# Kernel tuning notes

Hardware: AMD Instinct MI355X
Metric: run time of the kernel (lower is better)

The kernel has to match this reference:

```python
import jax, jax.numpy as jnp
import numpy as np

N, E = 20000, 320000          # nodes, edges
R, B = 9, 9                   # num_relations, num_bases
IN, HID, OUT = 128, 256, 64   # feature dims
EPS = 1e-5                    # LayerNorm eps


def layer_norm(h, gamma, beta):
    mu = jnp.mean(h, axis=-1, keepdims=True)
    var = jnp.var(h, axis=-1, keepdims=True)
    return (h - mu) * jax.lax.rsqrt(var + EPS) * gamma + beta


def rgcn_conv(x, src, dst, etype, bases, comp, root, bias, aggr):
    # basis decomposition: W_r = sum_b comp[r,b] * bases[b]
    W = jnp.einsum('rb,bio->rio', comp, bases)          # [R, in, out]
    xW = jnp.einsum('ni,rio->rno', x, W)                # [R, N, out]
    msg = xW[etype, src]                                # [E, out] gather per edge
    if aggr == 'max':
        agg = jax.ops.segment_max(msg, dst, num_segments=N)
        agg = jnp.where(jnp.isfinite(agg), agg, 0.0)    # empty segments -> 0
    else:
        agg = jax.ops.segment_sum(msg, dst, num_segments=N)
    return agg + x @ root + bias


def setup_inputs() -> dict:
    key = jax.random.key(0)
    ks = jax.random.split(key, 12)
    rn = lambda k, s, sc=0.05: jax.random.normal(k, s, jnp.float32) * sc
    return {
        'x': jax.random.normal(ks[0], (N, IN), jnp.float32),
        'edge_index': jax.random.randint(ks[1], (2, E), 0, N),
        'edge_type': jax.random.randint(ks[2], (E,), 0, R),
        # conv1 params
        'bases1': rn(ks[3], (B, IN, HID)),
        'comp1': rn(ks[4], (R, B), 0.3),
        'root1': rn(ks[5], (IN, HID)),
        'bias1': jnp.zeros((HID,), jnp.float32),
        'g1': jnp.ones((HID,), jnp.float32),
        'b1': jnp.zeros((HID,), jnp.float32),
        # conv2 params
        'bases2': rn(ks[6], (B, HID, OUT)),
        'comp2': rn(ks[7], (R, B), 0.3),
        'root2': rn(ks[8], (HID, OUT)),
        'bias2': jnp.zeros((OUT,), jnp.float32),
        'g2': jnp.ones((OUT,), jnp.float32),
        'b2': jnp.zeros((OUT,), jnp.float32),
    }


def reference(x, edge_index, edge_type, bases1, comp1, root1, bias1, g1, b1,
              bases2, comp2, root2, bias2, g2, b2):
    src, dst = edge_index[0], edge_index[1]
    h = rgcn_conv(x, src, dst, edge_type, bases1, comp1, root1, bias1, 'max')
    h = jax.nn.relu(layer_norm(h, g1, b1))
    # eval mode: edge dropout and feature dropout are identity
    h = rgcn_conv(h, src, dst, edge_type, bases2, comp2, root2, bias2, 'add')
    h = layer_norm(h, g2, b2)
    return jax.nn.log_softmax(h, axis=1)
```

## Files before the change

### kernel.cpp

```cpp
#include <hip/hip_runtime.h>
#include <math.h>

#define NN 20000
#define NE 320000
#define NREL 9
#define NBASES 9
#define D_IN 128
#define D_HID 256
#define D_OUT 64
#define LN_EPS 1e-5f

#define N1 (NREL * D_HID + D_HID)
#define N2 (NREL * D_OUT + D_OUT)
#define NBLK ((NN + 255) / 256)

typedef __attribute__((ext_vector_type(8))) short bf16x8;
typedef __attribute__((ext_vector_type(4))) float f32x4;
typedef __attribute__((ext_vector_type(4))) unsigned int u32x4;

__device__ inline ushort f2b(float f) {
    unsigned u = __float_as_uint(f);
    return (ushort)((u + 0x7FFFu + ((u >> 16) & 1u)) >> 16);
}
__device__ inline float b2f(ushort h) { return __uint_as_float(((unsigned)h) << 16); }
__device__ inline float b2f_lo(unsigned u) { return __uint_as_float(u << 16); }
__device__ inline float b2f_hi(unsigned u) { return __uint_as_float(u & 0xffff0000u); }
__device__ inline unsigned pack2bf(float f0, float f1) {
    return (unsigned)f2b(f0) | ((unsigned)f2b(f1) << 16);
}

__global__ __launch_bounds__(256) void prep_all(
    const float* __restrict__ bases1, const float* __restrict__ comp1, const float* __restrict__ root1,
    const float* __restrict__ bases2, const float* __restrict__ comp2, const float* __restrict__ root2,
    const float* __restrict__ x, const int* __restrict__ dst,
    ushort* __restrict__ w1t, ushort* __restrict__ w2t, ushort* __restrict__ xbf,
    int* __restrict__ deg)
{
    const int SZW1 = D_IN * D_HID;
    const int SZW2 = D_HID * D_OUT;
    const int SZX4 = NN * D_IN / 4;
    int tid = blockIdx.x * 256 + threadIdx.x;
    if (tid < SZW1) {
        int o = tid & (D_HID - 1), k = tid >> 8;
        float acc[NREL];
        #pragma unroll
        for (int r = 0; r < NREL; r++) acc[r] = 0.f;
        #pragma unroll
        for (int b = 0; b < NBASES; b++) {
            float bs = bases1[(b * D_IN + k) * D_HID + o];
            #pragma unroll
            for (int r = 0; r < NREL; r++) acc[r] += comp1[r * NBASES + b] * bs;
        }
        #pragma unroll
        for (int r = 0; r < NREL; r++)
            w1t[(r * D_HID + o) * D_IN + k] = f2b(acc[r]);
        w1t[(NREL * D_HID + o) * D_IN + k] = f2b(root1[k * D_HID + o]);
    } else if (tid < SZW1 + SZW2) {
        int j = tid - SZW1;
        int o = j & (D_OUT - 1), k = j >> 6;
        float acc[NREL];
        #pragma unroll
        for (int r = 0; r < NREL; r++) acc[r] = 0.f;
        #pragma unroll
        for (int b = 0; b < NBASES; b++) {
            float bs = bases2[(b * D_HID + k) * D_OUT + o];
            #pragma unroll
            for (int r = 0; r < NREL; r++) acc[r] += comp2[r * NBASES + b] * bs;
        }
        #pragma unroll
        for (int r = 0; r < NREL; r++)
            w2t[(r * D_OUT + o) * D_HID + k] = f2b(acc[r]);
        w2t[(NREL * D_OUT + o) * D_HID + k] = f2b(root2[k * D_OUT + o]);
    } else if (tid < SZW1 + SZW2 + SZX4) {
        int j = tid - SZW1 - SZW2;
        float4 v = *(const float4*)&x[(size_t)j * 4];
        ushort4 o;
        o.x = f2b(v.x); o.y = f2b(v.y); o.z = f2b(v.z); o.w = f2b(v.w);
        *(ushort4*)&xbf[(size_t)j * 4] = o;
    } else if (tid < SZW1 + SZW2 + SZX4 + NE) {
        int e = tid - SZW1 - SZW2 - SZX4;
        atomicAdd(&deg[dst[e]], 1);
    }
}

__global__ __launch_bounds__(256) void scan_blk(
    const int* __restrict__ deg, int* __restrict__ local, int* __restrict__ bsum)
{
    __shared__ int wsum[4];
    int tid = threadIdx.x, lane = tid & 63, w = tid >> 6;
    int i = blockIdx.x * 256 + tid;
    int v = (i < NN) ? deg[i] : 0;
    int x = v;
    #pragma unroll
    for (int d = 1; d < 64; d <<= 1) {
        int y = __shfl_up(x, d, 64);
        if (lane >= d) x += y;
    }
    if (lane == 63) wsum[w] = x;
    __syncthreads();
    int woff = 0;
    for (int j = 0; j < w; j++) woff += wsum[j];
    if (i < NN) local[i] = woff + x - v;
    if (tid == 255) bsum[blockIdx.x] = woff + x;
}

__global__ __launch_bounds__(256) void scan_fin(
    const int* __restrict__ local, const int* __restrict__ bsum,
    int* __restrict__ offs, int* __restrict__ cursor)
{
    __shared__ int boff_s[NBLK];
    int tid = threadIdx.x;
    if (tid < 64) {
        int carry = 0;
        for (int base = 0; base < NBLK; base += 64) {
            int i = base + tid;
            int v = (i < NBLK) ? bsum[i] : 0;
            int x = v;
            #pragma unroll
            for (int d = 1; d < 64; d <<= 1) {
                int y = __shfl_up(x, d, 64);
                if (tid >= d) x += y;
            }
            if (i < NBLK) boff_s[i] = carry + x - v;
            carry += __shfl(x, 63, 64);
        }
    }
    __syncthreads();
    int i = blockIdx.x * 256 + tid;
    if (i < NN) {
        int o = local[i] + boff_s[i >> 8];
        offs[i] = o;
        cursor[i] = o;
    }
    if (i == NN) offs[NN] = NE;
}

__global__ __launch_bounds__(256) void scatter_ep(
    const int* __restrict__ src, const int* __restrict__ dst, const int* __restrict__ etype,
    int* __restrict__ cursor, int* __restrict__ ep1)
{
    int e = blockIdx.x * 256 + threadIdx.x;
    if (e >= NE) return;
    int d = dst[e];
    int s = src[e], r = etype[e];
    int pos = atomicAdd(&cursor[d], 1);
    ep1[pos] = s * N1 + r * D_HID;
}

__global__ __launch_bounds__(512) void gemm_bf16(
    const ushort* __restrict__ A, const ushort* __restrict__ Bt, ushort* __restrict__ C,
    int M, int N, int K)
{
    __shared__ ushort smem[16384];
    ushort* Asb = smem;
    ushort* Bsb = smem + 8192;

    int nwg = gridDim.x * gridDim.y;
    int o = blockIdx.y * gridDim.x + blockIdx.x;
    int q = nwg >> 3, r = nwg & 7;
    int xcd = o & 7, idx = o >> 3;
    int wk = (xcd < r ? xcd * (q + 1) : r * (q + 1) + (xcd - r) * q) + idx;
    int bx = wk % gridDim.x, by = wk / gridDim.x;

    int tid = threadIdx.x;
    int lane = tid & 63, w = tid >> 6;
    int wm = w >> 1, wn = w & 1;
    int row0 = by * 128, col0 = bx * 128;

    int r0 = tid >> 2, q0 = tid & 3;
    int mrw = r0 & 15, gw = r0 >> 4;
    int sw = q0 * 16 + ((mrw + 2 * q0) & 15);
    int lo = (gw * 64 + sw) * 8;
    int arow = min(row0 + r0, M - 1);
    const ushort* gA = &A[(size_t)arow * K + q0 * 8];
    const ushort* gB = &Bt[(size_t)(col0 + r0) * K + q0 * 8];

    int mr = lane & 15, kq = lane >> 4;
    int inner = (kq * 16 + ((mr + 2 * kq) & 15)) * 8;

    f32x4 acc[2][4];
    #pragma unroll
    for (int mt = 0; mt < 2; mt++)
        #pragma unroll
        for (int nt = 0; nt < 4; nt++)
            acc[mt][nt] = (f32x4){0.f, 0.f, 0.f, 0.f};

    {
        bf16x8 a0 = *(const bf16x8*)gA;
        bf16x8 b0 = *(const bf16x8*)gB;
        *(bf16x8*)&Asb[lo] = a0;
        *(bf16x8*)&Bsb[lo] = b0;
    }

    const int NC = K >> 5;
    for (int c = 0; c < NC; c++) {
        __syncthreads();
        int cur = c & 1, nxt = cur ^ 1;
        bf16x8 a0, b0;
        bool more = (c + 1 < NC);
        if (more) {
            gA += 32; gB += 32;
            a0 = *(const bf16x8*)gA;
            b0 = *(const bf16x8*)gB;
        }

        bf16x8 af[2], bfr[4];
        #pragma unroll
        for (int mt = 0; mt < 2; mt++)
            af[mt] = *(const bf16x8*)&Asb[cur * 4096 + ((wm * 2 + mt) * 64) * 8 + inner];
        #pragma unroll
        for (int nt = 0; nt < 4; nt++)
            bfr[nt] = *(const bf16x8*)&Bsb[cur * 4096 + ((wn * 4 + nt) * 64) * 8 + inner];
        #pragma unroll
        for (int mt = 0; mt < 2; mt++)
            #pragma unroll
            for (int nt = 0; nt < 4; nt++)
                acc[mt][nt] = __builtin_amdgcn_mfma_f32_16x16x32_bf16(
                    bfr[nt], af[mt], acc[mt][nt], 0, 0, 0);

        if (more) {
            *(bf16x8*)&Asb[nxt * 4096 + lo] = a0;
            *(bf16x8*)&Bsb[nxt * 4096 + lo] = b0;
        }
    }

    __syncthreads();
    int qo = lane >> 4, cm = lane & 15;
    #pragma unroll
    for (int mt = 0; mt < 2; mt++) {
        int row = wm * 32 + mt * 16 + cm;
        int sx = (row & 7) << 3;
        #pragma unroll
        for (int nt = 0; nt < 4; nt++) {
            int colT = wn * 64 + nt * 16 + qo * 4;
            uint2 oo;
            oo.x = pack2bf(acc[mt][nt][0], acc[mt][nt][1]);
            oo.y = pack2bf(acc[mt][nt][2], acc[mt][nt][3]);
            *(uint2*)&smem[(row * 128 + colT) ^ sx] = oo;
        }
    }
    __syncthreads();
    #pragma unroll
    for (int i = 0; i < 4; i++) {
        int rr = (tid >> 4) + i * 32;
        int seg = tid & 15;
        u32x4 val = *(const u32x4*)&smem[(rr * 128 + seg * 8) ^ ((rr & 7) << 3)];
        int gr = row0 + rr;
        if (gr < M)
            __builtin_nontemporal_store(val, (u32x4*)&C[(size_t)gr * N + col0 + seg * 8]);
    }
}

__global__ __launch_bounds__(256) void gather1(
    const ushort* __restrict__ xw1, const int* __restrict__ offs, const int* __restrict__ ep1,
    const float* __restrict__ bias, const float* __restrict__ g, const float* __restrict__ b,
    ushort* __restrict__ hout)
{
    int n = blockIdx.x * 4 + (threadIdx.x >> 6);
    if (n >= NN) return;
    int lane = threadIdx.x & 63;
    int hf = lane >> 5;
    int il = lane & 31;
    int cbase = il * 8;
    int e0 = __builtin_amdgcn_readfirstlane(offs[n]);
    int e1 = __builtin_amdgcn_readfirstlane(offs[n + 1]);

    float m[8];
    #pragma unroll
    for (int k = 0; k < 8; k++) m[k] = -INFINITY;

    int e = e0;
    for (; e + 8 <= e1; e += 8) {
        int p[4];
        #pragma unroll
        for (int j = 0; j < 4; j++) p[j] = ep1[e + 2 * j + hf];
        uint4 v[4];
        #pragma unroll
        for (int j = 0; j < 4; j++) v[j] = *(const uint4*)&xw1[(size_t)p[j] + cbase];
        #pragma unroll
        for (int j = 0; j < 4; j++) {
            m[0] = fmaxf(m[0], b2f_lo(v[j].x)); m[1] = fmaxf(m[1], b2f_hi(v[j].x));
            m[2] = fmaxf(m[2], b2f_lo(v[j].y)); m[3] = fmaxf(m[3], b2f_hi(v[j].y));
            m[4] = fmaxf(m[4], b2f_lo(v[j].z)); m[5] = fmaxf(m[5], b2f_hi(v[j].z));
            m[6] = fmaxf(m[6], b2f_lo(v[j].w)); m[7] = fmaxf(m[7], b2f_hi(v[j].w));
        }
    }
    for (; e < e1; e += 2) {
        int ee = min(e + hf, e1 - 1);
        int p = ep1[ee];
        uint4 v = *(const uint4*)&xw1[(size_t)p + cbase];
        m[0] = fmaxf(m[0], b2f_lo(v.x)); m[1] = fmaxf(m[1], b2f_hi(v.x));
        m[2] = fmaxf(m[2], b2f_lo(v.y)); m[3] = fmaxf(m[3], b2f_hi(v.y));
        m[4] = fmaxf(m[4], b2f_lo(v.z)); m[5] = fmaxf(m[5], b2f_hi(v.z));
        m[6] = fmaxf(m[6], b2f_lo(v.w)); m[7] = fmaxf(m[7], b2f_hi(v.w));
    }
    #pragma unroll
    for (int k = 0; k < 8; k++) m[k] = fmaxf(m[k], __shfl_xor(m[k], 32, 64));
    if (e1 == e0) {
        #pragma unroll
        for (int k = 0; k < 8; k++) m[k] = 0.f;
    }

    int c0 = cbase + hf * 4;
    float a0 = hf ? m[4] : m[0];
    float a1 = hf ? m[5] : m[1];
    float a2 = hf ? m[6] : m[2];
    float a3 = hf ? m[7] : m[3];

    ushort4 rt = *(const ushort4*)&xw1[(size_t)n * N1 + NREL * D_HID + c0];
    float t0 = a0 + b2f(rt.x) + bias[c0 + 0];
    float t1 = a1 + b2f(rt.y) + bias[c0 + 1];
    float t2 = a2 + b2f(rt.z) + bias[c0 + 2];
    float t3 = a3 + b2f(rt.w) + bias[c0 + 3];

    float s = t0 + t1 + t2 + t3;
    float s2 = t0 * t0 + t1 * t1 + t2 * t2 + t3 * t3;
    #pragma unroll
    for (int mm = 32; mm >= 1; mm >>= 1) {
        s  += __shfl_xor(s,  mm, 64);
        s2 += __shfl_xor(s2, mm, 64);
    }
    float mu = s * (1.f / D_HID);
    float var = s2 * (1.f / D_HID) - mu * mu;
    float rs = rsqrtf(var + LN_EPS);

    ushort4 o;
    o.x = f2b(fmaxf((t0 - mu) * rs * g[c0 + 0] + b[c0 + 0], 0.f));
    o.y = f2b(fmaxf((t1 - mu) * rs * g[c0 + 1] + b[c0 + 1], 0.f));
    o.z = f2b(fmaxf((t2 - mu) * rs * g[c0 + 2] + b[c0 + 2], 0.f));
    o.w = f2b(fmaxf((t3 - mu) * rs * g[c0 + 3] + b[c0 + 3], 0.f));
    *(ushort4*)&hout[(size_t)n * D_HID + c0] = o;
}

__global__ __launch_bounds__(256) void gather2(
    const ushort* __restrict__ xw2, const int* __restrict__ offs, const int* __restrict__ ep1,
    const float* __restrict__ bias, const float* __restrict__ g, const float* __restrict__ b,
    float* __restrict__ out)
{
    int n = blockIdx.x * 4 + (threadIdx.x >> 6);
    if (n >= NN) return;
    int lane = threadIdx.x & 63;
    int q = lane >> 4;
    int ql = lane & 15;
    int cb = ql * 4;
    int e0 = __builtin_amdgcn_readfirstlane(offs[n]);
    int e1 = __builtin_amdgcn_readfirstlane(offs[n + 1]);

    float s0 = 0.f, s1 = 0.f, s2p = 0.f, s3 = 0.f;
    int e = e0;
    for (; e + 8 <= e1; e += 8) {
        int pa = ep1[e + q] >> 2;
        int pb = ep1[e + 4 + q] >> 2;
        uint2 va = *(const uint2*)&xw2[(size_t)pa + cb];
        uint2 vb = *(const uint2*)&xw2[(size_t)pb + cb];
        s0 += b2f_lo(va.x) + b2f_lo(vb.x);
        s1 += b2f_hi(va.x) + b2f_hi(vb.x);
        s2p += b2f_lo(va.y) + b2f_lo(vb.y);
        s3 += b2f_hi(va.y) + b2f_hi(vb.y);
    }
    for (; e < e1; e += 4) {
        if (e + q < e1) {
            int p = ep1[e + q] >> 2;
            uint2 v = *(const uint2*)&xw2[(size_t)p + cb];
            s0 += b2f_lo(v.x); s1 += b2f_hi(v.x);
            s2p += b2f_lo(v.y); s3 += b2f_hi(v.y);
        }
    }
    s0 += __shfl_xor(s0, 16, 64); s0 += __shfl_xor(s0, 32, 64);
    s1 += __shfl_xor(s1, 16, 64); s1 += __shfl_xor(s1, 32, 64);
    s2p += __shfl_xor(s2p, 16, 64); s2p += __shfl_xor(s2p, 32, 64);
    s3 += __shfl_xor(s3, 16, 64); s3 += __shfl_xor(s3, 32, 64);

    int c = cb + q;
    float agg = (q == 0) ? s0 : (q == 1) ? s1 : (q == 2) ? s2p : s3;
    float v = agg + b2f(xw2[(size_t)n * N2 + NREL * D_OUT + c]) + bias[c];

    float sm = v, sq = v * v;
    #pragma unroll
    for (int mm = 32; mm >= 1; mm >>= 1) {
        sm += __shfl_xor(sm, mm, 64);
        sq += __shfl_xor(sq, mm, 64);
    }
    float mu = sm * (1.f / D_OUT);
    float var = sq * (1.f / D_OUT) - mu * mu;
    float y = (v - mu) * rsqrtf(var + LN_EPS) * g[c] + b[c];

    float mx = y;
    #pragma unroll
    for (int mm = 32; mm >= 1; mm >>= 1) mx = fmaxf(mx, __shfl_xor(mx, mm, 64));
    float ex = __expf(y - mx);
    float se = ex;
    #pragma unroll
    for (int mm = 32; mm >= 1; mm >>= 1) se += __shfl_xor(se, mm, 64);
    out[(size_t)n * D_OUT + c] = y - mx - logf(se);
}

extern "C" void kernel_launch(void* const* d_in, const int* in_sizes, int n_in,
                              void* d_out, int out_size, void* d_ws, size_t ws_size,
                              hipStream_t stream)
{
    const float* x      = (const float*)d_in[0];
    const int*   eidx   = (const int*)  d_in[1];
    const int*   etype  = (const int*)  d_in[2];
    const float* bases1 = (const float*)d_in[3];
    const float* comp1  = (const float*)d_in[4];
    const float* root1  = (const float*)d_in[5];
    const float* bias1  = (const float*)d_in[6];
    const float* g1     = (const float*)d_in[7];
    const float* b1     = (const float*)d_in[8];
    const float* bases2 = (const float*)d_in[9];
    const float* comp2  = (const float*)d_in[10];
    const float* root2  = (const float*)d_in[11];
    const float* bias2  = (const float*)d_in[12];
    const float* g2     = (const float*)d_in[13];
    const float* b2     = (const float*)d_in[14];

    const int* src = eidx;
    const int* dst = eidx + NE;

    char* p = (char*)d_ws;
    auto alloc = [&](size_t bytes) -> char* {
        char* r = p;
        p += (bytes + 255) & ~(size_t)255;
        return r;
    };
    ushort* xbf    = (ushort*)alloc((size_t)NN * D_IN * 2);
    ushort* w1t    = (ushort*)alloc((size_t)N1 * D_IN * 2);
    ushort* w2t    = (ushort*)alloc((size_t)N2 * D_HID * 2);
    ushort* xw1    = (ushort*)alloc((size_t)NN * N1 * 2);
    ushort* xw2    = (ushort*)alloc((size_t)NN * N2 * 2);
    ushort* h      = (ushort*)alloc((size_t)NN * D_HID * 2);
    int*    deg    = (int*)   alloc((size_t)NN * 4);
    int*    local  = (int*)   alloc((size_t)NN * 4);
    int*    bsum   = (int*)   alloc((size_t)NBLK * 4);
    int*    offs   = (int*)   alloc((size_t)(NN + 1) * 4);
    int*    cursor = (int*)   alloc((size_t)NN * 4);
    int*    ep1    = (int*)   alloc((size_t)NE * 4);

    hipMemsetAsync(deg, 0, (size_t)NN * 4, stream);
    const int SZP = D_IN * D_HID + D_HID * D_OUT + NN * D_IN / 4 + NE;
    prep_all<<<(SZP + 255) / 256, 256, 0, stream>>>(
        bases1, comp1, root1, bases2, comp2, root2, x, dst, w1t, w2t, xbf, deg);

    scan_blk<<<NBLK, 256, 0, stream>>>(deg, local, bsum);
    scan_fin<<<NBLK, 256, 0, stream>>>(local, bsum, offs, cursor);
    scatter_ep<<<(NE + 255) / 256, 256, 0, stream>>>(src, dst, etype, cursor, ep1);

    gemm_bf16<<<dim3(N1 / 128, (NN + 127) / 128), 512, 0, stream>>>(xbf, w1t, xw1, NN, N1, D_IN);
    gather1<<<(NN + 3) / 4, 256, 0, stream>>>(xw1, offs, ep1, bias1, g1, b1, h);

    gemm_bf16<<<dim3(N2 / 128, (NN + 127) / 128), 512, 0, stream>>>(h, w2t, xw2, NN, N2, D_HID);
    gather2<<<(NN + 3) / 4, 256, 0, stream>>>(xw2, offs, ep1, bias2, g2, b2, (float*)d_out);
}
```

Measured before the change: 222.5 us.

## Deepen gather unrolling and drop XCD remap and nontemporal stores in GEMM

Adds 16-edge unrolled main loops to both gather kernels, so each lane keeps more independent row loads in flight and hides gather latency better, at the cost of extra registers. The GEMM loses its XCD-aware workgroup remapping and writes its output with ordinary stores instead of nontemporal ones. Ordinary stores let the xW output stay in cache for the gathers that read it next, but dropping the remap can hurt L2 locality across XCDs.

```diff
diff --git a/kernel.cpp b/kernel.cpp
--- a/kernel.cpp
+++ b/kernel.cpp
@@ -16,7 +16,6 @@
 
 typedef __attribute__((ext_vector_type(8))) short bf16x8;
 typedef __attribute__((ext_vector_type(4))) float f32x4;
-typedef __attribute__((ext_vector_type(4))) unsigned int u32x4;
 
 __device__ inline ushort f2b(float f) {
     unsigned u = __float_as_uint(f);
@@ -155,17 +154,10 @@
     ushort* Asb = smem;
     ushort* Bsb = smem + 8192;
 
-    int nwg = gridDim.x * gridDim.y;
-    int o = blockIdx.y * gridDim.x + blockIdx.x;
-    int q = nwg >> 3, r = nwg & 7;
-    int xcd = o & 7, idx = o >> 3;
-    int wk = (xcd < r ? xcd * (q + 1) : r * (q + 1) + (xcd - r) * q) + idx;
-    int bx = wk % gridDim.x, by = wk / gridDim.x;
-
     int tid = threadIdx.x;
     int lane = tid & 63, w = tid >> 6;
     int wm = w >> 1, wn = w & 1;
-    int row0 = by * 128, col0 = bx * 128;
+    int row0 = blockIdx.y * 128, col0 = blockIdx.x * 128;
 
     int r0 = tid >> 2, q0 = tid & 3;
     int mrw = r0 & 15, gw = r0 >> 4;
@@ -244,10 +236,10 @@
     for (int i = 0; i < 4; i++) {
         int rr = (tid >> 4) + i * 32;
         int seg = tid & 15;
-        u32x4 val = *(const u32x4*)&smem[(rr * 128 + seg * 8) ^ ((rr & 7) << 3)];
+        uint4 val = *(const uint4*)&smem[(rr * 128 + seg * 8) ^ ((rr & 7) << 3)];
         int gr = row0 + rr;
         if (gr < M)
-            __builtin_nontemporal_store(val, (u32x4*)&C[(size_t)gr * N + col0 + seg * 8]);
+            *(uint4*)&C[(size_t)gr * N + col0 + seg * 8] = val;
     }
 }
 
@@ -270,6 +262,21 @@
     for (int k = 0; k < 8; k++) m[k] = -INFINITY;
 
     int e = e0;
+    for (; e + 16 <= e1; e += 16) {
+        int p[8];
+        #pragma unroll
+        for (int j = 0; j < 8; j++) p[j] = ep1[e + 2 * j + hf];
+        uint4 v[8];
+        #pragma unroll
+        for (int j = 0; j < 8; j++) v[j] = *(const uint4*)&xw1[(size_t)p[j] + cbase];
+        #pragma unroll
+        for (int j = 0; j < 8; j++) {
+            m[0] = fmaxf(m[0], b2f_lo(v[j].x)); m[1] = fmaxf(m[1], b2f_hi(v[j].x));
+            m[2] = fmaxf(m[2], b2f_lo(v[j].y)); m[3] = fmaxf(m[3], b2f_hi(v[j].y));
+            m[4] = fmaxf(m[4], b2f_lo(v[j].z)); m[5] = fmaxf(m[5], b2f_hi(v[j].z));
+            m[6] = fmaxf(m[6], b2f_lo(v[j].w)); m[7] = fmaxf(m[7], b2f_hi(v[j].w));
+        }
+    }
     for (; e + 8 <= e1; e += 8) {
         int p[4];
         #pragma unroll
@@ -348,6 +355,19 @@
 
     float s0 = 0.f, s1 = 0.f, s2p = 0.f, s3 = 0.f;
     int e = e0;
+    for (; e + 16 <= e1; e += 16) {
+        int p[4];
+        #pragma unroll
+        for (int j = 0; j < 4; j++) p[j] = ep1[e + 4 * j + q] >> 2;
+        uint2 v[4];
+        #pragma unroll
+        for (int j = 0; j < 4; j++) v[j] = *(const uint2*)&xw2[(size_t)p[j] + cb];
+        #pragma unroll
+        for (int j = 0; j < 4; j++) {
+            s0 += b2f_lo(v[j].x); s1 += b2f_hi(v[j].x);
+            s2p += b2f_lo(v[j].y); s3 += b2f_hi(v[j].y);
+        }
+    }
     for (; e + 8 <= e1; e += 8) {
         int pa = ep1[e + q] >> 2;
         int pb = ep1[e + 4 + q] >> 2;
```

Result: no change. 220.9 us (-0.7%).
